# Kernel tuning notes

Measured on AMD Instinct MI355X. Metric: run time of the kernel, lower is better.

Reference implementation:

```python
import jax, jax.numpy as jnp
import numpy as np

N = 262144   # total ragged elements (batch * avg set size)
D = 256      # set feature dimension
B = 512      # number of sets
M = 1024     # max_set_size


def setup_inputs() -> dict:
    key = jax.random.key(0)
    k1, k2 = jax.random.split(key)
    src = jax.random.normal(k1, (N, D), dtype=jnp.float32)
    batch = jnp.sort(jax.random.randint(k2, (N,), 0, B).astype(jnp.int64))
    return {"src": src, "batch": batch, "num_sets": B, "max_set_size": M}


def reference(src, batch, num_sets, max_set_size):
    # Position of each element within its own set (batch is sorted).
    n = src.shape[0]
    counts = jax.ops.segment_sum(jnp.ones((n,), dtype=jnp.int32), batch,
                                 num_segments=num_sets)
    starts = jnp.cumsum(counts) - counts                 # exclusive prefix sum, [B]
    pos = jnp.arange(n, dtype=jnp.int32) - starts[batch]  # intra-set index, [N]

    # Scatter ragged rows into dense padded tensor; elements beyond
    # max_set_size are dropped (mode='drop'), matching truncating pad.
    padded = jnp.zeros((num_sets, max_set_size, src.shape[1]), dtype=src.dtype)
    padded = padded.at[batch, pos].set(src, mode="drop")

    mask = jnp.zeros((num_sets, max_set_size), dtype=bool)
    mask = mask.at[batch, pos].set(True, mode="drop")
    return padded, mask
```

## Files before the change

### kernel.cpp

```cpp
#include <hip/hip_runtime.h>

#define FEAT_D   256
#define MAX_M    1024
#define NSETS    512

typedef float f4 __attribute__((ext_vector_type(4)));

__global__ void k_starts(const int* __restrict__ batch, int n,
                         int* __restrict__ starts) {
    int b = blockIdx.x * blockDim.x + threadIdx.x;
    if (b > NSETS) return;
    int lo = 0, hi = n;
    while (lo < hi) {
        int mid = (lo + hi) >> 1;
        if (batch[mid] < b) lo = mid + 1; else hi = mid;
    }
    starts[b] = lo;
}

__global__ void k_gather(const f4* __restrict__ src4,
                         const int* __restrict__ starts,
                         f4* __restrict__ out4,
                         float* __restrict__ mask) {
    int tid  = blockIdx.x * blockDim.x + threadIdx.x;
    int row  = tid >> 6;
    int lane = tid & 63;
    int b = row >> 10;
    int m = row & (MAX_M - 1);
    int s   = starts[b];
    int cnt = starts[b + 1] - s;
    f4 v = (f4)(0.0f);
    bool valid = (m < cnt);
    if (valid)
        v = __builtin_nontemporal_load(&src4[(size_t)(s + m) * (FEAT_D / 4) + lane]);
    __builtin_nontemporal_store(v, &out4[(size_t)row * (FEAT_D / 4) + lane]);
    if (lane == 0)
        __builtin_nontemporal_store(valid ? 1.0f : 0.0f, &mask[row]);
}

extern "C" void kernel_launch(void* const* d_in, const int* in_sizes, int n_in,
                              void* d_out, int out_size, void* d_ws, size_t ws_size,
                              hipStream_t stream) {
    const float* src   = (const float*)d_in[0];
    const int*   batch = (const int*)d_in[1];
    int n = in_sizes[1];

    int* starts = (int*)d_ws;

    k_starts<<<(NSETS + 1 + 255) / 256, 256, 0, stream>>>(batch, n, starts);

    int total_rows = NSETS * MAX_M;
    float* mask = (float*)d_out + (size_t)NSETS * MAX_M * FEAT_D;
    k_gather<<<total_rows / 4, 256, 0, stream>>>(
        (const f4*)src, starts, (f4*)d_out, mask);
}
```

Measured before the change: 150.7 us.

## Assign 64 rows per wave with unrolled loop and vectorized mask writes

Changes the gather grid from one wave per output row to 2048 blocks where each wave copies 64 consecutive rows of a set in an 8-way unrolled loop. The per-set start and count are loaded once per block instead of once per row. Mask values are written as float4 by one quarter-block per set instead of one scalar per row. This cuts grid size and per-row index overhead, but leaves fewer waves in flight to hide memory latency on what is a bandwidth-bound copy.

```diff
diff --git a/kernel.cpp b/kernel.cpp
--- a/kernel.cpp
+++ b/kernel.cpp
@@ -18,24 +18,39 @@
     starts[b] = lo;
 }
 
-__global__ void k_gather(const f4* __restrict__ src4,
-                         const int* __restrict__ starts,
-                         f4* __restrict__ out4,
-                         float* __restrict__ mask) {
-    int tid  = blockIdx.x * blockDim.x + threadIdx.x;
-    int row  = tid >> 6;
-    int lane = tid & 63;
-    int b = row >> 10;
-    int m = row & (MAX_M - 1);
+__global__ void __launch_bounds__(256)
+k_gather(const f4* __restrict__ src4,
+         const int* __restrict__ starts,
+         f4* __restrict__ out4,
+         f4* __restrict__ mask4) {
+    int b = blockIdx.x >> 2;
+    int q = blockIdx.x & 3;
+    int wave = threadIdx.x >> 6;
+    int lane = threadIdx.x & 63;
     int s   = starts[b];
     int cnt = starts[b + 1] - s;
-    f4 v = (f4)(0.0f);
-    bool valid = (m < cnt);
-    if (valid)
-        v = __builtin_nontemporal_load(&src4[(size_t)(s + m) * (FEAT_D / 4) + lane]);
-    __builtin_nontemporal_store(v, &out4[(size_t)row * (FEAT_D / 4) + lane]);
-    if (lane == 0)
-        __builtin_nontemporal_store(valid ? 1.0f : 0.0f, &mask[row]);
+
+    int r0 = q * 256 + wave * 64;
+    const f4* ip = src4 + ((size_t)s + r0) * (FEAT_D / 4) + lane;
+    f4*       op = out4 + (((size_t)b << 10) + r0) * (FEAT_D / 4) + lane;
+
+    #pragma unroll 8
+    for (int j = 0; j < 64; ++j) {
+        f4 v = (f4)(0.0f);
+        if (r0 + j < cnt)
+            v = __builtin_nontemporal_load(ip + (size_t)j * (FEAT_D / 4));
+        __builtin_nontemporal_store(v, op + (size_t)j * (FEAT_D / 4));
+    }
+
+    if (q == 0) {
+        int t = threadIdx.x;
+        f4 mv;
+        mv[0] = (4 * t + 0) < cnt ? 1.0f : 0.0f;
+        mv[1] = (4 * t + 1) < cnt ? 1.0f : 0.0f;
+        mv[2] = (4 * t + 2) < cnt ? 1.0f : 0.0f;
+        mv[3] = (4 * t + 3) < cnt ? 1.0f : 0.0f;
+        __builtin_nontemporal_store(mv, &mask4[((size_t)b << 8) + t]);
+    }
 }
 
 extern "C" void kernel_launch(void* const* d_in, const int* in_sizes, int n_in,
@@ -49,8 +64,7 @@
 
     k_starts<<<(NSETS + 1 + 255) / 256, 256, 0, stream>>>(batch, n, starts);
 
-    int total_rows = NSETS * MAX_M;
-    float* mask = (float*)d_out + (size_t)NSETS * MAX_M * FEAT_D;
-    k_gather<<<total_rows / 4, 256, 0, stream>>>(
-        (const f4*)src, starts, (f4*)d_out, mask);
+    f4* mask4 = (f4*)((float*)d_out + (size_t)NSETS * MAX_M * FEAT_D);
+    k_gather<<<NSETS * 4, 256, 0, stream>>>(
+        (const f4*)src, starts, (f4*)d_out, mask4);
 }
```

After: 196.6 us. 30.5% more time.
